# Performance work log

Measured on AMD Instinct MI355X. Metric: run time of the kernel, lower is better.

## Reference

```python
import jax, jax.numpy as jnp
import numpy as np

IMAGE_W, IMAGE_H = 1024, 800
STRIDES = (8, 16, 32, 64, 128)
LEVEL_HW = ((100, 128), (50, 64), (25, 32), (13, 16), (7, 8))
TOP_N = 1000
MIN_SCORE = 0.01
NMS_THR = 0.6
MAX_DET = 100
NUM_CLASSES = 80
BATCH = 16


def _grid(h, w, stride, b):
    ys = (jnp.arange(h, dtype=jnp.float32) + 0.5) * stride
    xs = (jnp.arange(w, dtype=jnp.float32) + 0.5) * stride
    gx, gy = jnp.meshgrid(xs, ys)  # [h, w]
    pos = jnp.stack([gx, gy], axis=-1)  # [h, w, 2] = (x, y)
    return jnp.broadcast_to(pos, (b, h, w, 2))


def setup_inputs() -> dict:
    key = jax.random.key(0)
    inp = {}
    for i, ((h, w), s) in enumerate(zip(LEVEL_HW, STRIDES)):
        key, k1, k2, k3 = jax.random.split(key, 4)
        inp[f"cls{i}"] = jax.random.normal(k1, (BATCH, h, w, NUM_CLASSES), jnp.float32)
        # +3 so exp(reg) gives realistic ~20px box extents
        inp[f"reg{i}"] = jax.random.normal(k2, (BATCH, h, w, 4), jnp.float32) + 3.0
        inp[f"ctr{i}"] = jax.random.normal(k3, (BATCH, h, w, 1), jnp.float32)
        inp[f"pos{i}"] = _grid(h, w, s, BATCH)
    return inp


def _level_filter(cls, reg, ctr, pos):
    b = cls.shape[0]
    cls = jax.nn.sigmoid(cls).reshape(b, -1, NUM_CLASSES)
    reg = jnp.exp(reg).reshape(b, -1, 4)
    ctr = jax.nn.sigmoid(ctr).reshape(b, -1)
    pos = pos.reshape(b, -1, 2)
    scores = jnp.sqrt(jnp.max(cls, axis=2) * ctr)  # [b, n]
    classes = jnp.argmax(cls, axis=2)  # [b, n] int
    if scores.shape[1] >= TOP_N:
        scores, idx = jax.lax.top_k(scores, TOP_N)
        classes = jnp.take_along_axis(classes, idx, axis=1)
        reg = jnp.take_along_axis(reg, idx[..., None], axis=1)
        pos = jnp.take_along_axis(pos, idx[..., None], axis=1)
        cls = jnp.take_along_axis(cls, idx[..., None], axis=1)
    return scores, classes, reg, pos, cls


def _decode_boxes(reg, pos):
    # ltrb offsets -> x1y1x2y2, truncate to int (torch .int()), clamp to image
    xy_min = pos - reg[..., 0:2]
    xy_max = pos + reg[..., 2:4]
    bx = jnp.trunc(jnp.concatenate([xy_min, xy_max], axis=-1))
    x1 = jnp.maximum(bx[..., 0], 0.0)
    y1 = jnp.maximum(bx[..., 1], 0.0)
    x2 = jnp.minimum(bx[..., 2], IMAGE_W - 1.0)
    y2 = jnp.minimum(bx[..., 3], IMAGE_H - 1.0)
    return jnp.stack([x1, y1, x2, y2], axis=-1)


def _nms_image(scores, classes, boxes, clsp):
    valid = scores > MIN_SCORE
    order = jnp.argsort(jnp.where(valid, -scores, jnp.inf))  # valid, desc score first
    s = scores[order]
    c = classes[order].astype(jnp.float32)
    b = boxes[order]
    cp = clsp[order]
    v = valid[order]
    # pairwise IoU (keep/suppress decisions are not differentiated)
    bb = jax.lax.stop_gradient(b)
    area = (bb[:, 2] - bb[:, 0]) * (bb[:, 3] - bb[:, 1])
    lt = jnp.maximum(bb[:, None, :2], bb[None, :, :2])
    rb = jnp.minimum(bb[:, None, 2:], bb[None, :, 2:])
    wh = jnp.maximum(rb - lt, 0.0)
    inter = wh[..., 0] * wh[..., 1]
    iou = inter / (area[:, None] + area[None, :] - inter)
    n = s.shape[0]
    idxs = jnp.arange(n)

    def body(i, keep):
        sup = keep[i] & (iou[i] > NMS_THR) & (idxs > i)
        return keep & ~sup

    keep = jax.lax.fori_loop(0, n, body, v)
    rank = jnp.cumsum(keep) - 1
    slot = jnp.where(keep & (rank < MAX_DET), rank, MAX_DET)  # MAX_DET -> dropped
    out_s = jnp.full((MAX_DET,), -1.0, jnp.float32).at[slot].set(s, mode="drop")
    out_c = jnp.full((MAX_DET,), -1.0, jnp.float32).at[slot].set(c, mode="drop")
    out_b = jnp.full((MAX_DET, 4), -1.0, jnp.float32).at[slot].set(b, mode="drop")
    out_cp = jnp.full((MAX_DET, NUM_CLASSES), -1.0, jnp.float32).at[slot].set(cp, mode="drop")
    return out_s, out_c, out_b, out_cp


def reference(cls0, cls1, cls2, cls3, cls4, reg0, reg1, reg2, reg3, reg4,
              ctr0, ctr1, ctr2, ctr3, ctr4, pos0, pos1, pos2, pos3, pos4):
    clss = [cls0, cls1, cls2, cls3, cls4]
    regs = [reg0, reg1, reg2, reg3, reg4]
    ctrs = [ctr0, ctr1, ctr2, ctr3, ctr4]
    poss = [pos0, pos1, pos2, pos3, pos4]
    parts = [_level_filter(c, r, t, p) for c, r, t, p in zip(clss, regs, ctrs, poss)]
    scores = jnp.concatenate([p[0] for p in parts], axis=1)
    classes = jnp.concatenate([p[1] for p in parts], axis=1)
    reg = jnp.concatenate([p[2] for p in parts], axis=1)
    pos = jnp.concatenate([p[3] for p in parts], axis=1)
    clsp = jnp.concatenate([p[4] for p in parts], axis=1)
    boxes = _decode_boxes(reg, pos)
    return jax.vmap(_nms_image)(scores, classes, boxes, clsp)
```

## Files before the change

kernel.cpp:

```cpp
#include <hip/hip_runtime.h>
#include <math.h>

#define TOTAL_G 17064
#define BATCHN  16
#define ALLF    0xFFFFFFFFFFFFFFFFull
#define INVALID_HI 0xC3DC28F5u

typedef unsigned long long u64;
typedef unsigned int u32;
typedef unsigned short u16;

#define KEYS0_OFF   0
#define KEYS1_OFF   1638400
#define KEYS234_OFF 2048000
#define CLSI_OFF    2187264
#define NC_OFF      2733312
#define T512_OFF    2733824
#define KR_OFF      2733952
#define MSK_OFF     2799488
#define SLOTK_OFF   3323776

struct Ptrs {
  const float *cls0,*cls1,*cls2,*cls3,*cls4;
  const float *reg0,*reg1,*reg2,*reg3,*reg4;
  const float *ctr0,*ctr1,*ctr2,*ctr3,*ctr4;
  const float *pos0,*pos1,*pos2,*pos3,*pos4;
  char *ws;
};

__device__ __forceinline__ float sigd(float x) {
  return (float)(1.0 / (1.0 + exp(-(double)x)));
}
__device__ __forceinline__ float dexp(float x) {
  return (float)exp((double)x);
}
__device__ __forceinline__ void levinfo(int gid, int& lev, int& idx, int& nl) {
  if      (gid < 12800) { lev=0; idx=gid;        nl=12800; }
  else if (gid < 16000) { lev=1; idx=gid-12800;  nl=3200;  }
  else if (gid < 16800) { lev=2; idx=gid-16000;  nl=800;   }
  else if (gid < 17008) { lev=3; idx=gid-16800;  nl=208;   }
  else                  { lev=4; idx=gid-17008;  nl=56;    }
}

__device__ __forceinline__ u64* krank_of(char* ws, int b) {
  return (u64*)(ws + KR_OFF + (size_t)b * 4096);
}
__device__ __forceinline__ u64* msk_of(char* ws, int b) {
  return (u64*)(ws + MSK_OFF + (size_t)b * 32768);
}
__device__ __forceinline__ u64* slotkey_of(char* ws, int b) {
  return (u64*)(ws + SLOTK_OFF + (size_t)b * 800);
}

__device__ __forceinline__ float4 decode_box(const Ptrs& P, int b, int gid) {
  int lev, idx, nl; levinfo(gid, lev, idx, nl);
  const float *rp, *pp;
  if      (lev == 0) { rp = P.reg0; pp = P.pos0; }
  else if (lev == 1) { rp = P.reg1; pp = P.pos1; }
  else if (lev == 2) { rp = P.reg2; pp = P.pos2; }
  else if (lev == 3) { rp = P.reg3; pp = P.pos3; }
  else               { rp = P.reg4; pp = P.pos4; }
  float4 rv = *(const float4*)(rp + (size_t)(b * nl + idx) * 4);
  float2 pv = *(const float2*)(pp + (size_t)(b * nl + idx) * 2);
  float e0 = dexp(rv.x), e1 = dexp(rv.y), e2 = dexp(rv.z), e3 = dexp(rv.w);
  float x1 = truncf(pv.x - e0), y1 = truncf(pv.y - e1);
  float x2 = truncf(pv.x + e2), y2 = truncf(pv.y + e3);
  x1 = fmaxf(x1, 0.0f); y1 = fmaxf(y1, 0.0f);
  x2 = fminf(x2, 1023.0f); y2 = fminf(y2, 799.0f);
  return make_float4(x1, y1, x2, y2);
}

__global__ __launch_bounds__(256) void k_score(Ptrs P) {
  __shared__ float4 sk4[64 * 20];
  int b = blockIdx.y;
  int tid = threadIdx.x;
  int p0 = blockIdx.x * 64;

  #pragma unroll
  for (int it = 0; it < 5; ++it) {
    int t4 = it * 256 + tid;
    int g = p0 + t4 / 20;
    if (g < TOTAL_G) {
      int sub = t4 - (t4 / 20) * 20;
      int lev, idx, nl; levinfo(g, lev, idx, nl);
      const float* clsb;
      if      (lev == 0) clsb = P.cls0;
      else if (lev == 1) clsb = P.cls1;
      else if (lev == 2) clsb = P.cls2;
      else if (lev == 3) clsb = P.cls3;
      else               clsb = P.cls4;
      sk4[t4] = ((const float4*)(clsb + (size_t)(b * nl + idx) * 80))[sub];
    }
  }
  __syncthreads();

  int lp = tid >> 2, q = tid & 3;
  int g = p0 + lp;
  if (g >= TOTAL_G) return;

  const float4* my4 = &sk4[lp * 20 + q * 5];
  float m = -INFINITY, m2 = -INFINITY; int mi = 0;
  #pragma unroll
  for (int k = 0; k < 5; ++k) {
    float4 v = my4[k];
    int base = q * 20 + 4 * k;
    if (v.x > m) { m2 = m; m = v.x; mi = base+0; } else if (v.x > m2) m2 = v.x;
    if (v.y > m) { m2 = m; m = v.y; mi = base+1; } else if (v.y > m2) m2 = v.y;
    if (v.z > m) { m2 = m; m = v.z; mi = base+2; } else if (v.z > m2) m2 = v.z;
    if (v.w > m) { m2 = m; m = v.w; mi = base+3; } else if (v.w > m2) m2 = v.w;
  }
  #pragma unroll
  for (int xw = 1; xw <= 2; xw <<= 1) {
    float om  = __shfl_xor(m,  xw);
    float om2 = __shfl_xor(m2, xw);
    int   omi = __shfl_xor(mi, xw);
    bool take = (om > m) || (om == m && omi < mi);
    float lm  = take ? m : om;
    float wm2 = take ? om2 : m2;
    if (take) { m = om; mi = omi; }
    m2 = fmaxf(lm, wm2);
  }

  float thr = fminf(m - 1e-3f, 9.0f);
  float pmax; int ci;
  if (m2 >= thr) {
    float pv = -1.0f; int pi = 0x7fffffff;
    #pragma unroll 1
    for (int k = 0; k < 5; ++k) {
      float4 v = my4[k];
      float xs[4] = {v.x, v.y, v.z, v.w};
      #pragma unroll
      for (int e = 0; e < 4; ++e) {
        if (xs[e] >= thr) {
          float p = sigd(xs[e]);
          if (p > pv) { pv = p; pi = q * 20 + 4 * k + e; }
        }
      }
    }
    #pragma unroll
    for (int xw = 1; xw <= 2; xw <<= 1) {
      float ov = __shfl_xor(pv, xw);
      int   oi = __shfl_xor(pi, xw);
      if (ov > pv || (ov == pv && oi < pi)) { pv = ov; pi = oi; }
    }
    pmax = pv; ci = pi;
  } else {
    pmax = sigd(m); ci = mi;
  }

  if (q == 0) {
    int lev, idx, nl; levinfo(g, lev, idx, nl);
    const float* ctrb;
    if      (lev == 0) ctrb = P.ctr0;
    else if (lev == 1) ctrb = P.ctr1;
    else if (lev == 2) ctrb = P.ctr2;
    else if (lev == 3) ctrb = P.ctr3;
    else               ctrb = P.ctr4;
    float tc = ctrb[(size_t)b * nl + idx];
    float csig = sigd(tc);
    float prod = pmax * csig;
    float s = (float)sqrt((double)prod);
    ((u16*)(P.ws + CLSI_OFF))[(size_t)b * TOTAL_G + g] = (u16)ci;
    unsigned hi = ~__float_as_uint(s);
    u64 key = ((u64)hi << 15) | (unsigned)g;
    if      (lev == 0) ((u64*)(P.ws + KEYS0_OFF))  [(size_t)b * 12800 + idx] = key;
    else if (lev == 1) ((u64*)(P.ws + KEYS1_OFF))  [(size_t)b * 3200  + idx] = key;
    else               ((u64*)(P.ws + KEYS234_OFF))[(size_t)b * 1088  + (g - 16000)] = key;
  }
}

__device__ __forceinline__ u64 loadkey(const Ptrs& P, int b, int u) {
  if (u < 12800) return ((const u64*)(P.ws + KEYS0_OFF))  [(size_t)b * 12800 + u];
  if (u < 16000) return ((const u64*)(P.ws + KEYS1_OFF))  [(size_t)b * 3200  + (u - 12800)];
  return               ((const u64*)(P.ws + KEYS234_OFF))[(size_t)b * 1088  + (u - 16000)];
}
__device__ __forceinline__ bool keep_pred(u64 k, int u, u64 T0, u64 T1) {
  bool valid = (u32)(k >> 15) < INVALID_HI;
  bool sel = (u < 12800) ? (k <= T0) : ((u < 16000) ? (k <= T1) : true);
  return valid && sel;
}

__global__ __launch_bounds__(1024) void k_mask(Ptrs P) {
  __shared__ union USh {
    u32 H[4][4096];
    struct { float4 sbox[512]; u64 smaskR[4096]; u16 parts[1024]; } M;
  } U;
  __shared__ u64 skey[512];
  __shared__ u16 srank[512];
  __shared__ int wbase[272];
  __shared__ int sN5;
  __shared__ u64 sBoundary;
  int qi = blockIdx.x, b = blockIdx.y;
  int tid = threadIdx.x, wid = tid >> 6, lane = tid & 63;
  char* ws = P.ws;

  for (int i = tid; i < 4 * 4096; i += 1024) (&U.H[0][0])[i] = 0;
  __syncthreads();
  for (int u = tid; u < TOTAL_G; u += 1024) {
    u64 k = loadkey(P, b, u);
    if ((u32)(k >> 15) < INVALID_HI)
      atomicAdd(&U.H[wid & 3][(u32)(k >> 29) & 0xFFF], 1u);
  }
  __syncthreads();
  for (int i = tid; i < 4096; i += 1024) {
    u32 v = U.H[0][i] + U.H[1][i] + U.H[2][i] + U.H[3][i];
    U.H[0][i] = v;
  }
  __syncthreads();
  if (wid == 0) {
    u32 ssum = 0;
    #pragma unroll 8
    for (int i = 0; i < 64; ++i) {
      int ii = (i + lane) & 63;
      ssum += U.H[0][(lane << 6) + ii];
    }
    u32 inc = ssum;
    for (int o = 1; o < 64; o <<= 1) { u32 v = __shfl_up(inc, o); if (lane >= o) inc += v; }
    u64 ball = __ballot(inc >= 512u);
    if (!ball) {
      if (lane == 0) sBoundary = ((u64)INVALID_HI << 15);
    } else {
      int Wq = __ffsll(ball) - 1;
      u32 cumBefore = __shfl(inc - ssum, Wq);
      u32 v2 = U.H[0][(Wq << 6) + lane];
      u32 inc2 = v2;
      for (int o = 1; o < 64; o <<= 1) { u32 x = __shfl_up(inc2, o); if (lane >= o) inc2 += x; }
      u64 ball2 = __ballot(cumBefore + inc2 >= 512u);
      int l2 = __ffsll(ball2) - 1;
      if (lane == 0) {
        int d = (Wq << 6) + l2;
        sBoundary = (48ull << 41) | ((u64)d << 29);
      }
    }
  }
  __syncthreads();
  u64 Boundary = sBoundary;
  if (qi == 0 && tid == 0) ((u64*)(ws + T512_OFF))[b] = Boundary - 1;

  for (int it = 0; it < 17; ++it) {
    int u = it * 1024 + tid;
    bool keep5 = false;
    if (u < TOTAL_G) {
      u64 k = loadkey(P, b, u);
      keep5 = ((u32)(k >> 15) < INVALID_HI) && (k < Boundary);
    }
    u64 bal = __ballot(keep5);
    if (lane == 0) wbase[it * 16 + wid] = __popcll(bal);
  }
  __syncthreads();
  if (wid == 0) {
    int carry = 0;
    for (int base = 0; base < 272; base += 64) {
      int idx = base + lane;
      int v = (idx < 272) ? wbase[idx] : 0;
      int inc = v;
      for (int o = 1; o < 64; o <<= 1) { int x = __shfl_up(inc, o); if (lane >= o) inc += x; }
      if (idx < 272) wbase[idx] = inc - v + carry;
      carry += __shfl(inc, 63);
    }
    if (lane == 0) sN5 = carry;
  }
  __syncthreads();
  int n512 = sN5;
  if (qi == 0 && tid == 0) ((int*)(ws + NC_OFF))[16 + b] = n512;

  for (int it = 0; it < 17; ++it) {
    int u = it * 1024 + tid;
    bool keep5 = false; u64 k = 0;
    if (u < TOTAL_G) {
      k = loadkey(P, b, u);
      keep5 = ((u32)(k >> 15) < INVALID_HI) && (k < Boundary);
    }
    u64 bal = __ballot(keep5);
    int pos = wbase[it * 16 + wid] + __popcll(bal & ((1ull << lane) - 1ull));
    if (keep5) skey[pos] = k;
  }
  __syncthreads();

  if (tid < 512) {
    if (tid < n512) {
      U.M.sbox[tid] = decode_box(P, b, (int)(skey[tid] & 0x7FFF));
    } else {
      skey[tid] = (ALLF - 511) + (u64)tid;
      U.M.sbox[tid] = make_float4(-1e30f, -1e30f, -1e30f, -1e30f);
    }
  }
  for (int i = tid; i < 512 * 8; i += 1024) U.M.smaskR[i] = 0ull;
  __syncthreads();

  {
    int t2 = tid & 511, half = tid >> 9;
    u64 mykey = skey[t2];
    int jb = half << 8, cnt = 0;
    #pragma unroll 4
    for (int j = jb; j < jb + 256; ++j) cnt += (skey[j] < mykey) ? 1 : 0;
    U.M.parts[tid] = (u16)cnt;
  }
  __syncthreads();
  if (tid < 512) srank[tid] = (u16)(U.M.parts[tid] + U.M.parts[tid + 512]);
  __syncthreads();

  int i = qi * 128 + (tid >> 3);
  int w = tid & 7;
  float4 bi = U.M.sbox[i];
  u64 ki = skey[i];
  int ri = srank[i];
  float ia = (bi.z - bi.x) * (bi.w - bi.y);
  #pragma unroll 8
  for (int bj = 0; bj < 64; ++bj) {
    int jj = (bj + w) & 63;
    int j = (w << 6) | jj;
    u64 kj = skey[j];
    if (ki < kj) {
      float4 bj4 = U.M.sbox[j];
      float ja  = (bj4.z - bj4.x) * (bj4.w - bj4.y);
      float ltx = fmaxf(bi.x, bj4.x), lty = fmaxf(bi.y, bj4.y);
      float rbx = fminf(bi.z, bj4.z), rby = fminf(bi.w, bj4.w);
      float wv = fmaxf(rbx - ltx, 0.0f), hv = fmaxf(rby - lty, 0.0f);
      float inter = wv * hv;
      float iou = inter / (ia + ja - inter);
      if (iou > 0.6f) {
        int rj = srank[j];
        atomicOr(&U.M.smaskR[ri * 8 + (rj >> 6)], 1ull << (rj & 63));
      }
    }
  }
  __syncthreads();

  {
    int il = tid >> 3, ww = tid & 7;
    int ig = qi * 128 + il;
    if (ig < n512) {
      int r = srank[ig];
      msk_of(ws, b)[r * 8 + ww] = U.M.smaskR[r * 8 + ww];
      if (ww == 0) krank_of(ws, b)[r] = skey[ig];
    }
  }
}

__device__ u64 select256(const u64* keys, int n, int t0, u32* hist, u64* shP, int* shT) {
  u64 Pfx = 3; int t = t0;
  const int SS[4] = {33, 21, 9, 0};
  const int WW[4] = {12, 12, 12, 9};
  for (int p = 0; p < 4; ++p) {
    int s = SS[p], wb = WW[p];
    u32 dmask = (1u << wb) - 1u;
    for (int i = threadIdx.x; i < 4096; i += 256) hist[i] = 0;
    __syncthreads();
    for (int i = threadIdx.x; i < n; i += 256) {
      u64 k = keys[i];
      if ((k >> (s + wb)) == Pfx) atomicAdd(&hist[(u32)(k >> s) & dmask], 1u);
    }
    __syncthreads();
    if (threadIdx.x < 64) {
      int lane = threadIdx.x;
      u32 ssum = 0;
      for (int i = 0; i < 64; ++i) ssum += hist[(lane << 6) + ((i + lane) & 63)];
      u32 inc = ssum;
      for (int o = 1; o < 64; o <<= 1) { u32 v = __shfl_up(inc, o); if (lane >= o) inc += v; }
      u64 ball = __ballot(inc >= (u32)t);
      int Wq = __ffsll(ball) - 1;
      u32 cumBefore = __shfl(inc - ssum, Wq);
      u32 v2 = hist[(Wq << 6) + lane];
      u32 inc2 = v2;
      for (int o = 1; o < 64; o <<= 1) { u32 x = __shfl_up(inc2, o); if (lane >= o) inc2 += x; }
      u64 ball2 = __ballot(cumBefore + inc2 >= (u32)t);
      int l2 = __ffsll(ball2) - 1;
      u32 cumB2 = __shfl(cumBefore + inc2 - v2, l2);
      if (lane == 0) { *shP = (Pfx << wb) | (u32)((Wq << 6) + l2); *shT = t - (int)cumB2; }
    }
    __syncthreads();
    Pfx = *shP; t = *shT;
    __syncthreads();
  }
  return Pfx;
}

__global__ __launch_bounds__(256) void k_reduce(Ptrs P) {
  __shared__ u64 smask[4096];
  __shared__ u32 keeplist[100];
  __shared__ int keptS;
  __shared__ u64 liveC[267];
  __shared__ union UF {
    u32 hist[4096];
    struct { u64 pk[256]; int pc[256]; float4 fkb[100]; } F;
  } UF_;
  __shared__ u64 shP; __shared__ int shT;
  __shared__ u64 bk; __shared__ int bc2;

  int b = blockIdx.x;
  int tid = threadIdx.x;
  char* ws = P.ws;
  int n512 = ((int*)(ws + NC_OFF))[16 + b];
  const u64* kr = krank_of(ws, b);

  const u64* gmask = msk_of(ws, b);
  for (int t = tid; t < 4096; t += 256) smask[t] = gmask[t];
  __syncthreads();

  if (tid < 64) {
    int lane = tid;
    u64 lw = 0;
    if (lane < 8) {
      int lo = lane << 6;
      int c = n512 - lo; if (c < 0) c = 0; if (c > 64) c = 64;
      lw = (c >= 64) ? ALLF : ((c > 0) ? ((1ull << c) - 1ull) : 0ull);
    }
    int kept = 0;
    while (kept < 100) {
      bool nz = (lane < 8) && (lw != 0ull);
      u64 bal = __ballot(nz);
      if (!bal) break;
      int W = __ffsll(bal) - 1;
      u64 wv = __shfl(lw, W);
      int bit = __ffsll(wv) - 1;
      int i = (W << 6) + bit;
      if (lane == 0) keeplist[kept] = (u32)i;
      kept++;
      if (lane == W) lw &= ~(1ull << bit);
      if (kept == 100) break;
      if (lane < 8) lw &= ~smask[i * 8 + lane];
    }
    if (lane == 0) keptS = kept;
  }
  __syncthreads();
  int kept = keptS;
  int keptW = kept;

  if (kept < 100) {
    u64 T0 = select256((const u64*)(ws + KEYS0_OFF) + (size_t)b * 12800, 12800, 1000,
                       UF_.hist, &shP, &shT);
    u64 T1 = select256((const u64*)(ws + KEYS1_OFF) + (size_t)b * 3200, 3200, 1000,
                       UF_.hist, &shP, &shT);
    u64 T512 = ((u64*)(ws + T512_OFF))[b];
    for (int w = tid; w < 267; w += 256) {
      int lo = w << 6;
      u64 m = 0;
      for (int e = 0; e < 64; ++e) {
        int u = lo + e;
        if (u < TOTAL_G) {
          u64 k = loadkey(P, b, u);
          if (keep_pred(k, u, T0, T1) && k > T512) m |= (1ull << e);
        }
      }
      liveC[w] = m;
    }
    if (tid < kept) UF_.F.fkb[tid] = decode_box(P, b, (int)(kr[keeplist[tid]] & 0x7FFF));
    __syncthreads();

    for (int k2 = 0; k2 < kept; ++k2) {
      float4 bi = UF_.F.fkb[k2];
      float ia = (bi.z - bi.x) * (bi.w - bi.y);
      for (int u = tid; u < TOTAL_G; u += 256) {
        if (!((liveC[u >> 6] >> (u & 63)) & 1ull)) continue;
        float4 bj4 = decode_box(P, b, u);
        float ja  = (bj4.z - bj4.x) * (bj4.w - bj4.y);
        float ltx = fmaxf(bi.x, bj4.x), lty = fmaxf(bi.y, bj4.y);
        float rbx = fminf(bi.z, bj4.z), rby = fminf(bi.w, bj4.w);
        float wv = fmaxf(rbx - ltx, 0.0f), hv = fmaxf(rby - lty, 0.0f);
        float inter = wv * hv;
        float iou = inter / (ia + ja - inter);
        if (iou > 0.6f) atomicAnd(&liveC[u >> 6], ~(1ull << (u & 63)));
      }
    }
    __syncthreads();

    while (kept < 100) {
      u64 mymin = ALLF; int myc = -1;
      for (int u = tid; u < TOTAL_G; u += 256) {
        if (!((liveC[u >> 6] >> (u & 63)) & 1ull)) continue;
        u64 k = loadkey(P, b, u);
        if (k < mymin) { mymin = k; myc = u; }
      }
      UF_.F.pk[tid] = mymin; UF_.F.pc[tid] = myc;
      __syncthreads();
      if (tid < 64) {
        u64 m = UF_.F.pk[tid]; int c0 = UF_.F.pc[tid];
        #pragma unroll
        for (int o = 64; o < 256; o += 64)
          if (UF_.F.pk[tid + o] < m) { m = UF_.F.pk[tid + o]; c0 = UF_.F.pc[tid + o]; }
        for (int o = 32; o > 0; o >>= 1) {
          u64 om = __shfl_down(m, o); int oc = __shfl_down(c0, o);
          if (om < m) { m = om; c0 = oc; }
        }
        if (tid == 0) { bk = m; bc2 = c0; }
      }
      __syncthreads();
      if (bk == ALLF) break;
      int cs = bc2;
      if (tid == 0) {
        slotkey_of(ws, b)[kept] = bk;
        atomicAnd(&liveC[cs >> 6], ~(1ull << (cs & 63)));
      }
      __syncthreads();
      kept++;
      if (kept == 100) break;
      float4 bi = decode_box(P, b, cs);
      float ia = (bi.z - bi.x) * (bi.w - bi.y);
      for (int u = tid; u < TOTAL_G; u += 256) {
        if (!((liveC[u >> 6] >> (u & 63)) & 1ull)) continue;
        float4 bj4 = decode_box(P, b, u);
        float ja  = (bj4.z - bj4.x) * (bj4.w - bj4.y);
        float ltx = fmaxf(bi.x, bj4.x), lty = fmaxf(bi.y, bj4.y);
        float rbx = fminf(bi.z, bj4.z), rby = fminf(bi.w, bj4.w);
        float wv = fmaxf(rbx - ltx, 0.0f), hv = fmaxf(rby - lty, 0.0f);
        float inter = wv * hv;
        float iou = inter / (ia + ja - inter);
        if (iou > 0.6f) atomicAnd(&liveC[u >> 6], ~(1ull << (u & 63)));
      }
      __syncthreads();
    }
  }

  if (tid < 100) {
    if (tid < keptW)      slotkey_of(ws, b)[tid] = kr[keeplist[tid]];
    else if (tid >= kept) slotkey_of(ws, b)[tid] = ALLF;
  }
}

__global__ __launch_bounds__(256) void k_out(Ptrs P, float* out) {
  int b = blockIdx.x, part = blockIdx.y;
  int s0 = part * 10;
  int tid = threadIdx.x;
  const u64* skl = slotkey_of(P.ws, b);

  if (tid < 10) {
    int s = s0 + tid;
    u64 key = skl[s];
    float os = -1.0f, oc = -1.0f;
    float4 bx = make_float4(-1.0f, -1.0f, -1.0f, -1.0f);
    if (key != ALLF) {
      int gid = (int)(key & 0x7FFF);
      os = __uint_as_float(~(u32)(key >> 15));
      oc = (float)((u16*)(P.ws + CLSI_OFF))[(size_t)b * TOTAL_G + gid];
      bx = decode_box(P, b, gid);
    }
    out[b * 100 + s] = os;
    out[1600 + b * 100 + s] = oc;
    *(float4*)(out + 3200 + (size_t)(b * 100 + s) * 4) = bx;
  }

  for (int t = tid; t < 800; t += 256) {
    int sl = t / 80, k = t - sl * 80;
    int s = s0 + sl;
    u64 key = skl[s];
    float val = -1.0f;
    if (key != ALLF) {
      int gid = (int)(key & 0x7FFF);
      int lev, idx, nl; levinfo(gid, lev, idx, nl);
      const float* cp;
      if      (lev == 0) cp = P.cls0;
      else if (lev == 1) cp = P.cls1;
      else if (lev == 2) cp = P.cls2;
      else if (lev == 3) cp = P.cls3;
      else               cp = P.cls4;
      val = sigd(cp[(size_t)(b * nl + idx) * 80 + k]);
    }
    out[9600 + (size_t)(b * 100 + s) * 80 + k] = val;
  }
}

extern "C" void kernel_launch(void* const* d_in, const int* in_sizes, int n_in,
                              void* d_out, int out_size, void* d_ws, size_t ws_size,
                              hipStream_t stream) {
  (void)in_sizes; (void)n_in; (void)out_size; (void)ws_size;
  Ptrs P;
  P.cls0 = (const float*)d_in[0];  P.reg0 = (const float*)d_in[1];
  P.ctr0 = (const float*)d_in[2];  P.pos0 = (const float*)d_in[3];
  P.cls1 = (const float*)d_in[4];  P.reg1 = (const float*)d_in[5];
  P.ctr1 = (const float*)d_in[6];  P.pos1 = (const float*)d_in[7];
  P.cls2 = (const float*)d_in[8];  P.reg2 = (const float*)d_in[9];
  P.ctr2 = (const float*)d_in[10]; P.pos2 = (const float*)d_in[11];
  P.cls3 = (const float*)d_in[12]; P.reg3 = (const float*)d_in[13];
  P.ctr3 = (const float*)d_in[14]; P.pos3 = (const float*)d_in[15];
  P.cls4 = (const float*)d_in[16]; P.reg4 = (const float*)d_in[17];
  P.ctr4 = (const float*)d_in[18]; P.pos4 = (const float*)d_in[19];
  P.ws = (char*)d_ws;

  k_score<<<dim3(267, 16), 256, 0, stream>>>(P);
  k_mask<<<dim3(4, 16), 1024, 0, stream>>>(P);
  k_reduce<<<16, 256, 0, stream>>>(P);
  k_out<<<dim3(16, 10), 256, 0, stream>>>(P, (float*)d_out);
}
```

Before: 99.13 us.

## Build score histogram in k_score and split candidate selection into k_prep kernel

The per-image histogram of key prefixes moves into k_score as global atomics, so the select stage only loads a precomputed histogram. The threshold and compaction logic moves into a new k_prep kernel that runs once per image instead of being repeated by all four k_mask blocks, and it reads keys two at a time with vector loads. k_mask then only loads the 512 compacted keys. This removes redundant key scans, at the cost of an extra memset, an extra kernel launch, and contended global atomics.

```diff
diff --git a/kernel.cpp b/kernel.cpp
--- a/kernel.cpp
+++ b/kernel.cpp
@@ -19,6 +19,8 @@
 #define KR_OFF      2733952
 #define MSK_OFF     2799488
 #define SLOTK_OFF   3323776
+#define K512_OFF    3336576
+#define HIST_OFF    3402112
 
 struct Ptrs {
   const float *cls0,*cls1,*cls2,*cls3,*cls4;
@@ -50,6 +52,9 @@
 }
 __device__ __forceinline__ u64* slotkey_of(char* ws, int b) {
   return (u64*)(ws + SLOTK_OFF + (size_t)b * 800);
+}
+__device__ __forceinline__ u64* k512_of(char* ws, int b) {
+  return (u64*)(ws + K512_OFF + (size_t)b * 4096);
 }
 
 __device__ __forceinline__ float4 decode_box(const Ptrs& P, int b, int gid) {
@@ -166,6 +171,8 @@
     if      (lev == 0) ((u64*)(P.ws + KEYS0_OFF))  [(size_t)b * 12800 + idx] = key;
     else if (lev == 1) ((u64*)(P.ws + KEYS1_OFF))  [(size_t)b * 3200  + idx] = key;
     else               ((u64*)(P.ws + KEYS234_OFF))[(size_t)b * 1088  + (g - 16000)] = key;
+    if (hi < INVALID_HI)
+      atomicAdd(&((u32*)(P.ws + HIST_OFF))[b * 4096 + (u32)((key >> 29) & 0xFFF)], 1u);
   }
 }
 
@@ -174,45 +181,36 @@
   if (u < 16000) return ((const u64*)(P.ws + KEYS1_OFF))  [(size_t)b * 3200  + (u - 12800)];
   return               ((const u64*)(P.ws + KEYS234_OFF))[(size_t)b * 1088  + (u - 16000)];
 }
+__device__ __forceinline__ ulonglong2 loadkey2(const Ptrs& P, int b, int u) {
+  if (u < 12800) return *(const ulonglong2*)((const u64*)(P.ws + KEYS0_OFF)   + (size_t)b * 12800 + u);
+  if (u < 16000) return *(const ulonglong2*)((const u64*)(P.ws + KEYS1_OFF)   + (size_t)b * 3200  + (u - 12800));
+  return               *(const ulonglong2*)((const u64*)(P.ws + KEYS234_OFF) + (size_t)b * 1088  + (u - 16000));
+}
 __device__ __forceinline__ bool keep_pred(u64 k, int u, u64 T0, u64 T1) {
   bool valid = (u32)(k >> 15) < INVALID_HI;
   bool sel = (u < 12800) ? (k <= T0) : ((u < 16000) ? (k <= T1) : true);
   return valid && sel;
 }
 
-__global__ __launch_bounds__(1024) void k_mask(Ptrs P) {
-  __shared__ union USh {
-    u32 H[4][4096];
-    struct { float4 sbox[512]; u64 smaskR[4096]; u16 parts[1024]; } M;
-  } U;
-  __shared__ u64 skey[512];
-  __shared__ u16 srank[512];
-  __shared__ int wbase[272];
+__global__ __launch_bounds__(1024) void k_prep(Ptrs P) {
+  __shared__ u32 h[4096];
+  __shared__ int wbase[144];
+  __shared__ u64 sBoundary;
   __shared__ int sN5;
-  __shared__ u64 sBoundary;
-  int qi = blockIdx.x, b = blockIdx.y;
+  int b = blockIdx.x;
   int tid = threadIdx.x, wid = tid >> 6, lane = tid & 63;
   char* ws = P.ws;
 
-  for (int i = tid; i < 4 * 4096; i += 1024) (&U.H[0][0])[i] = 0;
-  __syncthreads();
-  for (int u = tid; u < TOTAL_G; u += 1024) {
-    u64 k = loadkey(P, b, u);
-    if ((u32)(k >> 15) < INVALID_HI)
-      atomicAdd(&U.H[wid & 3][(u32)(k >> 29) & 0xFFF], 1u);
-  }
-  __syncthreads();
-  for (int i = tid; i < 4096; i += 1024) {
-    u32 v = U.H[0][i] + U.H[1][i] + U.H[2][i] + U.H[3][i];
-    U.H[0][i] = v;
-  }
-  __syncthreads();
+  const u32* gh = (const u32*)(ws + HIST_OFF) + (size_t)b * 4096;
+  for (int i = tid; i < 4096; i += 1024) h[i] = gh[i];
+  __syncthreads();
+
   if (wid == 0) {
     u32 ssum = 0;
     #pragma unroll 8
     for (int i = 0; i < 64; ++i) {
       int ii = (i + lane) & 63;
-      ssum += U.H[0][(lane << 6) + ii];
+      ssum += h[(lane << 6) + ii];
     }
     u32 inc = ssum;
     for (int o = 1; o < 64; o <<= 1) { u32 v = __shfl_up(inc, o); if (lane >= o) inc += v; }
@@ -222,7 +220,7 @@
     } else {
       int Wq = __ffsll(ball) - 1;
       u32 cumBefore = __shfl(inc - ssum, Wq);
-      u32 v2 = U.H[0][(Wq << 6) + lane];
+      u32 v2 = h[(Wq << 6) + lane];
       u32 inc2 = v2;
       for (int o = 1; o < 64; o <<= 1) { u32 x = __shfl_up(inc2, o); if (lane >= o) inc2 += x; }
       u64 ball2 = __ballot(cumBefore + inc2 >= 512u);
@@ -235,57 +233,70 @@
   }
   __syncthreads();
   u64 Boundary = sBoundary;
-  if (qi == 0 && tid == 0) ((u64*)(ws + T512_OFF))[b] = Boundary - 1;
-
-  for (int it = 0; it < 17; ++it) {
-    int u = it * 1024 + tid;
-    bool keep5 = false;
-    if (u < TOTAL_G) {
-      u64 k = loadkey(P, b, u);
-      keep5 = ((u32)(k >> 15) < INVALID_HI) && (k < Boundary);
-    }
-    u64 bal = __ballot(keep5);
-    if (lane == 0) wbase[it * 16 + wid] = __popcll(bal);
+  if (tid == 0) ((u64*)(ws + T512_OFF))[b] = Boundary - 1;
+
+  for (int it = 0; it < 9; ++it) {
+    int u = it * 2048 + tid * 2;
+    ulonglong2 kk = loadkey2(P, b, u);
+    bool k0 = (u     < TOTAL_G) && ((u32)(kk.x >> 15) < INVALID_HI) && (kk.x < Boundary);
+    bool k1 = (u + 1 < TOTAL_G) && ((u32)(kk.y >> 15) < INVALID_HI) && (kk.y < Boundary);
+    u64 b0 = __ballot(k0), b1 = __ballot(k1);
+    if (lane == 0) wbase[it * 16 + wid] = __popcll(b0) + __popcll(b1);
   }
   __syncthreads();
   if (wid == 0) {
     int carry = 0;
-    for (int base = 0; base < 272; base += 64) {
+    for (int base = 0; base < 144; base += 64) {
       int idx = base + lane;
-      int v = (idx < 272) ? wbase[idx] : 0;
+      int v = (idx < 144) ? wbase[idx] : 0;
       int inc = v;
       for (int o = 1; o < 64; o <<= 1) { int x = __shfl_up(inc, o); if (lane >= o) inc += x; }
-      if (idx < 272) wbase[idx] = inc - v + carry;
+      if (idx < 144) wbase[idx] = inc - v + carry;
       carry += __shfl(inc, 63);
     }
     if (lane == 0) sN5 = carry;
   }
   __syncthreads();
-  int n512 = sN5;
-  if (qi == 0 && tid == 0) ((int*)(ws + NC_OFF))[16 + b] = n512;
-
-  for (int it = 0; it < 17; ++it) {
-    int u = it * 1024 + tid;
-    bool keep5 = false; u64 k = 0;
-    if (u < TOTAL_G) {
-      k = loadkey(P, b, u);
-      keep5 = ((u32)(k >> 15) < INVALID_HI) && (k < Boundary);
-    }
-    u64 bal = __ballot(keep5);
-    int pos = wbase[it * 16 + wid] + __popcll(bal & ((1ull << lane) - 1ull));
-    if (keep5) skey[pos] = k;
-  }
-  __syncthreads();
+  if (tid == 0) ((int*)(ws + NC_OFF))[16 + b] = sN5;
+
+  u64* k5 = k512_of(ws, b);
+  for (int it = 0; it < 9; ++it) {
+    int u = it * 2048 + tid * 2;
+    ulonglong2 kk = loadkey2(P, b, u);
+    bool k0 = (u     < TOTAL_G) && ((u32)(kk.x >> 15) < INVALID_HI) && (kk.x < Boundary);
+    bool k1 = (u + 1 < TOTAL_G) && ((u32)(kk.y >> 15) < INVALID_HI) && (kk.y < Boundary);
+    u64 b0 = __ballot(k0), b1 = __ballot(k1);
+    u64 lm = (1ull << lane) - 1ull;
+    int pos0 = wbase[it * 16 + wid] + __popcll(b0 & lm) + __popcll(b1 & lm);
+    int pos1 = pos0 + (k0 ? 1 : 0);
+    if (k0) k5[pos0] = kk.x;
+    if (k1) k5[pos1] = kk.y;
+  }
+}
+
+__global__ __launch_bounds__(1024) void k_mask(Ptrs P) {
+  __shared__ u64 skey[512];
+  __shared__ float4 sbox[512];
+  __shared__ u16 srank[512];
+  __shared__ u16 parts[1024];
+  __shared__ u64 smaskR[4096];
+  int qi = blockIdx.x, b = blockIdx.y;
+  int tid = threadIdx.x;
+  char* ws = P.ws;
+  int n512 = ((int*)(ws + NC_OFF))[16 + b];
+  const u64* k5 = k512_of(ws, b);
 
   if (tid < 512) {
     if (tid < n512) {
-      U.M.sbox[tid] = decode_box(P, b, (int)(skey[tid] & 0x7FFF));
+      u64 k = k5[tid];
+      skey[tid] = k;
+      sbox[tid] = decode_box(P, b, (int)(k & 0x7FFF));
     } else {
       skey[tid] = (ALLF - 511) + (u64)tid;
-      U.M.sbox[tid] = make_float4(-1e30f, -1e30f, -1e30f, -1e30f);
-    }
-  }
-  for (int i = tid; i < 512 * 8; i += 1024) U.M.smaskR[i] = 0ull;
+      sbox[tid] = make_float4(-1e30f, -1e30f, -1e30f, -1e30f);
+    }
+  }
+  for (int i = tid; i < 512 * 8; i += 1024) smaskR[i] = 0ull;
   __syncthreads();
 
   {
@@ -294,15 +305,15 @@
     int jb = half << 8, cnt = 0;
     #pragma unroll 4
     for (int j = jb; j < jb + 256; ++j) cnt += (skey[j] < mykey) ? 1 : 0;
-    U.M.parts[tid] = (u16)cnt;
-  }
-  __syncthreads();
-  if (tid < 512) srank[tid] = (u16)(U.M.parts[tid] + U.M.parts[tid + 512]);
+    parts[tid] = (u16)cnt;
+  }
+  __syncthreads();
+  if (tid < 512) srank[tid] = (u16)(parts[tid] + parts[tid + 512]);
   __syncthreads();
 
   int i = qi * 128 + (tid >> 3);
   int w = tid & 7;
-  float4 bi = U.M.sbox[i];
+  float4 bi = sbox[i];
   u64 ki = skey[i];
   int ri = srank[i];
   float ia = (bi.z - bi.x) * (bi.w - bi.y);
@@ -312,7 +323,7 @@
     int j = (w << 6) | jj;
     u64 kj = skey[j];
     if (ki < kj) {
-      float4 bj4 = U.M.sbox[j];
+      float4 bj4 = sbox[j];
       float ja  = (bj4.z - bj4.x) * (bj4.w - bj4.y);
       float ltx = fmaxf(bi.x, bj4.x), lty = fmaxf(bi.y, bj4.y);
       float rbx = fminf(bi.z, bj4.z), rby = fminf(bi.w, bj4.w);
@@ -321,7 +332,7 @@
       float iou = inter / (ia + ja - inter);
       if (iou > 0.6f) {
         int rj = srank[j];
-        atomicOr(&U.M.smaskR[ri * 8 + (rj >> 6)], 1ull << (rj & 63));
+        atomicOr(&smaskR[ri * 8 + (rj >> 6)], 1ull << (rj & 63));
       }
     }
   }
@@ -332,7 +343,7 @@
     int ig = qi * 128 + il;
     if (ig < n512) {
       int r = srank[ig];
-      msk_of(ws, b)[r * 8 + ww] = U.M.smaskR[r * 8 + ww];
+      msk_of(ws, b)[r * 8 + ww] = smaskR[r * 8 + ww];
       if (ww == 0) krank_of(ws, b)[r] = skey[ig];
     }
   }
@@ -577,7 +588,10 @@
   P.ctr4 = (const float*)d_in[18]; P.pos4 = (const float*)d_in[19];
   P.ws = (char*)d_ws;
 
+  (void)hipMemsetAsync((char*)d_ws + HIST_OFF, 0, 16 * 4096 * 4, stream);
+
   k_score<<<dim3(267, 16), 256, 0, stream>>>(P);
+  k_prep<<<16, 1024, 0, stream>>>(P);
   k_mask<<<dim3(4, 16), 1024, 0, stream>>>(P);
   k_reduce<<<16, 256, 0, stream>>>(P);
   k_out<<<dim3(16, 10), 256, 0, stream>>>(P, (float*)d_out);
```

After: 155.4 us. 1.57x slower.
